# Kernel optimization log

Hardware: AMD Instinct MI355X
Metric: run time of the kernel (lower is better)

The kernel has to match this reference:

```python
import jax, jax.numpy as jnp
import numpy as np

N_SPACE = 197  # spatial tokens (ViT-B/16: 196 patches + CLS)
T = 8          # frames, fixed by space_time_pos shape (197*8, dim)
H = 12         # heads


def setup_inputs() -> dict:
    key = jax.random.key(0)
    ks = jax.random.split(key, 8)
    dim = 768
    B = 8
    Nq = 1576
    scale = dim ** -0.5
    return {
        "s_x": jax.random.normal(ks[0], (N_SPACE, B * T, dim), jnp.float32),
        "t_x": jax.random.normal(ks[1], (B, Nq, dim), jnp.float32),
        "space_time_pos": scale * jax.random.normal(ks[2], (N_SPACE * T, dim), jnp.float32),
        "q_w": jax.random.normal(ks[3], (dim, dim), jnp.float32) * 0.02,
        "q_b": jnp.zeros((dim,), jnp.float32),
        "kv_w": jax.random.normal(ks[4], (2 * dim, dim), jnp.float32) * 0.02,
        "kv_b": jnp.zeros((2 * dim,), jnp.float32),
        "proj_w": jax.random.normal(ks[5], (dim, dim), jnp.float32) * 0.02,
        "proj_b": jnp.zeros((dim,), jnp.float32),
    }


def reference(s_x, t_x, space_time_pos, q_w, q_b, kv_w, kv_b, proj_w, proj_b):
    n, BT, dim = s_x.shape
    B, Nq, _ = t_x.shape
    t = BT // B
    head_dim = dim // H
    scale = head_dim ** -0.5

    # rearrange 'n (b t) d -> b (t n) d'
    s = s_x.reshape(n, B, t, dim).transpose(1, 2, 0, 3).reshape(B, t * n, dim)
    s = s + space_time_pos  # (B, t*n, dim)

    # Q from t_x, K/V from s
    q = t_x @ q_w.T + q_b                      # (B, Nq, dim)
    kv = s @ kv_w.T + kv_b                     # (B, t*n, 2*dim)
    Nk = t * n
    # 'b n (e h d) -> e b h n d'
    kv = kv.reshape(B, Nk, 2, H, head_dim).transpose(2, 0, 3, 1, 4)
    k, v = kv[0], kv[1]                        # (B, H, Nk, hd)
    q = q.reshape(B, Nq, H, head_dim).transpose(0, 2, 1, 3) * scale  # (B, H, Nq, hd)

    attn = jnp.einsum('bhqd,bhkd->bhqk', q, k)
    attn = jax.nn.softmax(attn, axis=-1)
    out = jnp.einsum('bhqk,bhkd->bhqd', attn, v)   # (B, H, Nq, hd)
    out = out.transpose(0, 2, 1, 3).reshape(B, Nq, dim)
    return out @ proj_w.T + proj_b
```

## Files before the change

kernel.cpp:

```cpp
#include <hip/hip_runtime.h>
#include <stdint.h>

#define NSPACE 197
#define TFRAMES 8
#define NH 12
#define DIM 768
#define HD 64
#define BATCH 8
#define NQ 1576
#define NK 1576
#define M_REAL 12608
#define M_PAD 12672
#define VT_LD 1600

typedef __attribute__((ext_vector_type(8))) short s16x8;
typedef __attribute__((ext_vector_type(4))) short s16x4;
typedef __attribute__((ext_vector_type(4))) float f32x4;

__device__ inline uint16_t f2bf(float f) {
    union { float f; uint32_t i; } c; c.f = f;
    uint32_t r = c.i + 0x7FFF + ((c.i >> 16) & 1);
    return (uint16_t)(r >> 16);
}

__device__ inline uint32_t cvtpk_bf16(float lo, float hi) {
    uint32_t r;
    asm("v_cvt_pk_bf16_f32 %0, %1, %2" : "=v"(r) : "v"(lo), "v"(hi));
    return r;
}

__device__ inline float exp2_raw(float x) { return __builtin_amdgcn_exp2f(x); }

__device__ inline void gld_lds16(const uint16_t* g, uint16_t* l) {
    __builtin_amdgcn_global_load_lds(
        (const __attribute__((address_space(1))) void*)g,
        (__attribute__((address_space(3))) void*)l,
        16, 0, 0);
}

#define FILLB 4752
#define CONVQ_B 288
#define CONVKV_B 576
__global__ void prep(const float* __restrict__ t_x, const float* __restrict__ s_x,
                     const float* __restrict__ pos,
                     const float* __restrict__ q_w, const float* __restrict__ kv_w,
                     uint16_t* __restrict__ x_pad, uint16_t* __restrict__ s_pad,
                     uint16_t* __restrict__ wq, uint16_t* __restrict__ wkv) {
    int bx = blockIdx.x, tid = threadIdx.x;
    if (bx < FILLB) {
        int chunk = bx * 256 + tid;
        size_t off = (size_t)chunk * 8;
        s16x8 o;
        if (off < (size_t)M_REAL * DIM) {
            float4 a = *(const float4*)(t_x + off);
            float4 b = *(const float4*)(t_x + off + 4);
            union { s16x8 v; uint32_t u[4]; } p;
            p.u[0] = cvtpk_bf16(a.x, a.y);
            p.u[1] = cvtpk_bf16(a.z, a.w);
            p.u[2] = cvtpk_bf16(b.x, b.y);
            p.u[3] = cvtpk_bf16(b.z, b.w);
            o = p.v;
        } else {
            for (int j = 0; j < 8; j++) o[j] = 0;
        }
        *(s16x8*)(x_pad + off) = o;
    } else if (bx < 2 * FILLB) {
        int chunk = (bx - FILLB) * 256 + tid;
        int i = chunk / (DIM / 8);
        int cc = chunk - i * (DIM / 8);
        int d0 = cc * 8;
        uint16_t* dst = s_pad + (size_t)i * DIM + d0;
        if (i >= M_REAL) {
            s16x8 z; for (int j = 0; j < 8; j++) z[j] = 0;
            *(s16x8*)dst = z;
            return;
        }
        int b = i / NK, rr = i - b * NK;
        int t_i = rr / NSPACE, n_i = rr - t_i * NSPACE;
        const float* src = s_x + ((size_t)(n_i * (BATCH * TFRAMES) + b * TFRAMES + t_i)) * DIM + d0;
        const float* ps = pos + (size_t)rr * DIM + d0;
        float4 a0 = *(const float4*)src;
        float4 a1 = *(const float4*)(src + 4);
        float4 p0 = *(const float4*)ps;
        float4 p1 = *(const float4*)(ps + 4);
        union { s16x8 v; uint32_t u[4]; } o;
        o.u[0] = cvtpk_bf16(a0.x + p0.x, a0.y + p0.y);
        o.u[1] = cvtpk_bf16(a0.z + p0.z, a0.w + p0.w);
        o.u[2] = cvtpk_bf16(a1.x + p1.x, a1.y + p1.y);
        o.u[3] = cvtpk_bf16(a1.z + p1.z, a1.w + p1.w);
        *(s16x8*)dst = o.v;
    } else if (bx < 2 * FILLB + CONVQ_B) {
        int chunk = (bx - 2 * FILLB) * 256 + tid;
        size_t off = (size_t)chunk * 8;
        float4 a = *(const float4*)(q_w + off);
        float4 b = *(const float4*)(q_w + off + 4);
        union { s16x8 v; uint32_t u[4]; } o;
        o.u[0] = cvtpk_bf16(a.x, a.y);
        o.u[1] = cvtpk_bf16(a.z, a.w);
        o.u[2] = cvtpk_bf16(b.x, b.y);
        o.u[3] = cvtpk_bf16(b.z, b.w);
        *(s16x8*)(wq + off) = o.v;
    } else {
        int chunk = (bx - 2 * FILLB - CONVQ_B) * 256 + tid;
        size_t off = (size_t)chunk * 8;
        float4 a = *(const float4*)(kv_w + off);
        float4 b = *(const float4*)(kv_w + off + 4);
        union { s16x8 v; uint32_t u[4]; } o;
        o.u[0] = cvtpk_bf16(a.x, a.y);
        o.u[1] = cvtpk_bf16(a.z, a.w);
        o.u[2] = cvtpk_bf16(b.x, b.y);
        o.u[3] = cvtpk_bf16(b.z, b.w);
        *(s16x8*)(wkv + off) = o.v;
    }
}

__global__ void conv_f2b(const float* __restrict__ src, uint16_t* __restrict__ dst, int n8) {
    int chunk = blockIdx.x * 256 + threadIdx.x;
    if (chunk >= n8) return;
    size_t off = (size_t)chunk * 8;
    float4 a = *(const float4*)(src + off);
    float4 b = *(const float4*)(src + off + 4);
    union { s16x8 v; uint32_t u[4]; } o;
    o.u[0] = cvtpk_bf16(a.x, a.y);
    o.u[1] = cvtpk_bf16(a.z, a.w);
    o.u[2] = cvtpk_bf16(b.x, b.y);
    o.u[3] = cvtpk_bf16(b.z, b.w);
    *(s16x8*)(dst + off) = o.v;
}

template <int MODE>
__global__ __launch_bounds__(256)
void gemm_bt(const uint16_t* __restrict__ A, const uint16_t* __restrict__ W,
             const float* __restrict__ bias,
             uint16_t* __restrict__ out0, uint16_t* __restrict__ out1,
             float* __restrict__ outf) {
    __shared__ uint16_t As[128 * 32];
    __shared__ uint16_t Bs[128 * 32];
    const int t = threadIdx.x;
    const int lane = t & 63, w = t >> 6;
    const int r16 = lane & 15, quad = lane >> 4;
    const int wm = w >> 1, wn = w & 1;
    const int m0 = blockIdx.y * 128;
    const int n0 = blockIdx.x * 128;

    const int srow = w * 32 + (lane >> 2);
    const int scol = (lane & 3) * 8;
    const uint16_t* Ag = A + (size_t)(m0 + srow) * DIM + scol;
    const uint16_t* Wg = W + (size_t)(n0 + srow) * DIM + scol;
    uint16_t* Asw = &As[w * 32 * 32];
    uint16_t* Bsw = &Bs[w * 32 * 32];

    f32x4 acc[4][4];
    for (int a = 0; a < 4; a++)
        for (int bb = 0; bb < 4; bb++)
            for (int r = 0; r < 4; r++) acc[a][bb][r] = 0.f;

    for (int kk = 0; kk < DIM; kk += 32) {
        gld_lds16(Ag + kk, Asw);
        gld_lds16(Ag + kk + (size_t)16 * DIM, Asw + 16 * 32);
        gld_lds16(Wg + kk, Bsw);
        gld_lds16(Wg + kk + (size_t)16 * DIM, Bsw + 16 * 32);
        __syncthreads();
        s16x8 af[4], bfr[4];
        for (int mt = 0; mt < 4; mt++)
            af[mt] = *(const s16x8*)&As[(wm * 64 + mt * 16 + r16) * 32 + quad * 8];
        for (int nt = 0; nt < 4; nt++)
            bfr[nt] = *(const s16x8*)&Bs[(wn * 64 + nt * 16 + r16) * 32 + quad * 8];
        for (int mt = 0; mt < 4; mt++)
            for (int nt = 0; nt < 4; nt++)
                acc[mt][nt] = __builtin_amdgcn_mfma_f32_16x16x32_bf16(af[mt], bfr[nt], acc[mt][nt], 0, 0, 0);
        __syncthreads();
    }

    for (int mt = 0; mt < 4; mt++)
        for (int nt = 0; nt < 4; nt++) {
            int col = n0 + wn * 64 + nt * 16 + r16;
            float bz = bias[col];
            int rowb = m0 + wm * 64 + mt * 16 + quad * 4;
            for (int r = 0; r < 4; r++) {
                int i = rowb + r;
                if (i >= M_REAL) continue;
                float v = acc[mt][nt][r] + bz;
                if (MODE == 0) {
                    int b = i / NQ, nq = i - b * NQ;
                    int h = col >> 6, d = col & 63;
                    out0[(size_t)(((b * NH + h) * NQ) + nq) * HD + d] = f2bf(v * 0.18033688011112042f);
                } else if (MODE == 1) {
                    int b = i / NK, nk = i - b * NK;
                    if (col < DIM) {
                        int h = col >> 6, d = col & 63;
                        out0[(size_t)(((b * NH + h) * NK) + nk) * HD + d] = f2bf(v);
                    } else {
                        int c2 = col - DIM;
                        int h = c2 >> 6, d = c2 & 63;
                        out1[(size_t)(((b * NH + h) * NK) + nk) * HD + d] = f2bf(v);
                    }
                } else {
                    outf[(size_t)i * DIM + col] = v;
                }
            }
        }
}

__global__ __launch_bounds__(256)
void transpose_v(const uint16_t* __restrict__ v, uint16_t* __restrict__ vt) {
    __shared__ uint16_t T[64 * 72];
    int tile = blockIdx.x, bh = blockIdx.y;
    int nk0 = tile * 64;
    const uint16_t* V = v + (size_t)bh * NK * HD;
    uint16_t* VT = vt + (size_t)bh * HD * VT_LD;
    int tid = threadIdx.x;
    int rr = tid >> 3;
    int c8 = (tid & 7) * 8;
    for (int p = 0; p < 2; p++) {
        int lr = p * 32 + rr;
        int nk = nk0 + lr;
        s16x8 val;
        if (nk < NK) val = *(const s16x8*)(V + (size_t)nk * HD + c8);
        else for (int j = 0; j < 8; j++) val[j] = 0;
        for (int j = 0; j < 8; j++)
            T[(c8 + j) * 72 + lr] = (uint16_t)val[j];
    }
    __syncthreads();
    for (int p = 0; p < 2; p++) {
        int d = p * 32 + rr;
        s16x8 o = *(const s16x8*)&T[d * 72 + c8];
        *(s16x8*)(VT + (size_t)d * VT_LD + nk0 + c8) = o;
    }
}

#define NITER 50
__global__ __launch_bounds__(256)
void flash_attn(const uint16_t* __restrict__ q_buf, const uint16_t* __restrict__ k_buf,
                const uint16_t* __restrict__ vt_buf, uint16_t* __restrict__ ao) {
    __shared__ uint16_t Kb[2][32 * 72];
    __shared__ uint16_t Vb[2][64 * 40];
    int h = blockIdx.y, b = blockIdx.z;
    int tid = threadIdx.x;
    int lane = tid & 63, w = tid >> 6;
    int r16 = lane & 15, quad = lane >> 4;
    size_t bh = (size_t)(b * NH + h);
    const uint16_t* Q = q_buf + bh * NQ * HD;
    const uint16_t* K = k_buf + bh * NK * HD;
    const uint16_t* VT = vt_buf + bh * HD * VT_LD;
    int q0 = blockIdx.x * 128 + w * 32;

    const int kg = tid >> 3;
    const int kc = (tid & 7) * 8;
    const int kslot = ((kg >> 3) << 2) + (kg & 3) + ((kg & 4) ? 16 : 0);
    const int vd = tid >> 2;
    const int vc = (tid & 3) * 8;
    const uint16_t* Kg = K + (size_t)kg * HD + kc;
    const uint16_t* Vg = VT + (size_t)vd * VT_LD + vc;
    uint16_t* Kw = &Kb[0][kslot * 72 + kc];
    uint16_t* Vw = &Vb[0][vd * 40 + vc];
    const int KBSZ = 32 * 72, VBSZ = 64 * 40;

    s16x8 qf[2][2];
    for (int m = 0; m < 2; m++) {
        int qrow = q0 + m * 16 + r16;
        if (qrow < NQ) {
            qf[m][0] = *(const s16x8*)(Q + (size_t)qrow * HD + quad * 8);
            qf[m][1] = *(const s16x8*)(Q + (size_t)qrow * HD + 32 + quad * 8);
        } else {
            for (int j = 0; j < 8; j++) { qf[m][0][j] = 0; qf[m][1][j] = 0; }
        }
    }

    f32x4 z4;
    for (int r = 0; r < 4; r++) z4[r] = 0.f;
    s16x8 ones;
    for (int j = 0; j < 8; j++) ones[j] = (short)0x3F80;

    f32x4 oT[2][4];
    f32x4 oLs[2];
    for (int m = 0; m < 2; m++) {
        for (int dt = 0; dt < 4; dt++)
            for (int r = 0; r < 4; r++) oT[m][dt][r] = 0.f;
        for (int r = 0; r < 4; r++) oLs[m][r] = 0.f;
    }

    {
        s16x8 kv = *(const s16x8*)Kg;
        s16x8 vv = *(const s16x8*)Vg;
        *(s16x8*)Kw = kv;
        *(s16x8*)Vw = vv;
    }
    __syncthreads();

    for (int it = 0; it < NITER - 1; it++) {
        int kb = it * 32;
        int cur = it & 1, nxt = cur ^ 1;
        s16x8 knv = *(const s16x8*)(Kg + (size_t)(kb + 32) * HD);
        s16x8 vnv = *(const s16x8*)(Vg + kb + 32);

        const uint16_t* Kc = &Kb[cur][0];
        const uint16_t* Vc = &Vb[cur][0];
        s16x8 kfA0 = *(const s16x8*)(Kc + r16 * 72 + quad * 8);
        s16x8 kfA1 = *(const s16x8*)(Kc + r16 * 72 + 32 + quad * 8);
        s16x8 kfB0 = *(const s16x8*)(Kc + (16 + r16) * 72 + quad * 8);
        s16x8 kfB1 = *(const s16x8*)(Kc + (16 + r16) * 72 + 32 + quad * 8);

        s16x8 pf[2];
        #pragma unroll
        for (int m = 0; m < 2; m++) {
            f32x4 sA = __builtin_amdgcn_mfma_f32_16x16x32_bf16(kfA0, qf[m][0], z4, 0, 0, 0);
            sA = __builtin_amdgcn_mfma_f32_16x16x32_bf16(kfA1, qf[m][1], sA, 0, 0, 0);
            f32x4 sB = __builtin_amdgcn_mfma_f32_16x16x32_bf16(kfB0, qf[m][0], z4, 0, 0, 0);
            sB = __builtin_amdgcn_mfma_f32_16x16x32_bf16(kfB1, qf[m][1], sB, 0, 0, 0);
            f32x4 pA, pB;
            #pragma unroll
            for (int r = 0; r < 4; r++) { pA[r] = exp2_raw(sA[r]); pB[r] = exp2_raw(sB[r]); }
            union { s16x8 v; uint32_t u[4]; } pk;
            pk.u[0] = cvtpk_bf16(pA[0], pA[1]);
            pk.u[1] = cvtpk_bf16(pA[2], pA[3]);
            pk.u[2] = cvtpk_bf16(pB[0], pB[1]);
            pk.u[3] = cvtpk_bf16(pB[2], pB[3]);
            pf[m] = pk.v;
        }
        #pragma unroll
        for (int dt = 0; dt < 4; dt++) {
            s16x8 vf = *(const s16x8*)(Vc + (dt * 16 + r16) * 40 + quad * 8);
            oT[0][dt] = __builtin_amdgcn_mfma_f32_16x16x32_bf16(vf, pf[0], oT[0][dt], 0, 0, 0);
            oT[1][dt] = __builtin_amdgcn_mfma_f32_16x16x32_bf16(vf, pf[1], oT[1][dt], 0, 0, 0);
        }
        oLs[0] = __builtin_amdgcn_mfma_f32_16x16x32_bf16(ones, pf[0], oLs[0], 0, 0, 0);
        oLs[1] = __builtin_amdgcn_mfma_f32_16x16x32_bf16(ones, pf[1], oLs[1], 0, 0, 0);
        *(s16x8*)(Kw + nxt * KBSZ) = knv;
        *(s16x8*)(Vw + nxt * VBSZ) = vnv;
        __syncthreads();
    }

    {
        const int it = NITER - 1;
        const int kb = it * 32;
        const int cur = it & 1;
        const uint16_t* Kc = &Kb[cur][0];
        const uint16_t* Vc = &Vb[cur][0];
        s16x8 kfA0 = *(const s16x8*)(Kc + r16 * 72 + quad * 8);
        s16x8 kfA1 = *(const s16x8*)(Kc + r16 * 72 + 32 + quad * 8);
        s16x8 kfB0 = *(const s16x8*)(Kc + (16 + r16) * 72 + quad * 8);
        s16x8 kfB1 = *(const s16x8*)(Kc + (16 + r16) * 72 + 32 + quad * 8);

        s16x8 pf[2];
        #pragma unroll
        for (int m = 0; m < 2; m++) {
            f32x4 sA = __builtin_amdgcn_mfma_f32_16x16x32_bf16(kfA0, qf[m][0], z4, 0, 0, 0);
            sA = __builtin_amdgcn_mfma_f32_16x16x32_bf16(kfA1, qf[m][1], sA, 0, 0, 0);
            f32x4 sB = __builtin_amdgcn_mfma_f32_16x16x32_bf16(kfB0, qf[m][0], z4, 0, 0, 0);
            sB = __builtin_amdgcn_mfma_f32_16x16x32_bf16(kfB1, qf[m][1], sB, 0, 0, 0);
            f32x4 pA, pB;
            #pragma unroll
            for (int r = 0; r < 4; r++) {
                pA[r] = (kb + quad * 8 + r < NK)     ? exp2_raw(sA[r]) : 0.f;
                pB[r] = (kb + quad * 8 + 4 + r < NK) ? exp2_raw(sB[r]) : 0.f;
            }
            union { s16x8 v; uint32_t u[4]; } pk;
            pk.u[0] = cvtpk_bf16(pA[0], pA[1]);
            pk.u[1] = cvtpk_bf16(pA[2], pA[3]);
            pk.u[2] = cvtpk_bf16(pB[0], pB[1]);
            pk.u[3] = cvtpk_bf16(pB[2], pB[3]);
            pf[m] = pk.v;
        }
        #pragma unroll
        for (int dt = 0; dt < 4; dt++) {
            s16x8 vf = *(const s16x8*)(Vc + (dt * 16 + r16) * 40 + quad * 8);
            oT[0][dt] = __builtin_amdgcn_mfma_f32_16x16x32_bf16(vf, pf[0], oT[0][dt], 0, 0, 0);
            oT[1][dt] = __builtin_amdgcn_mfma_f32_16x16x32_bf16(vf, pf[1], oT[1][dt], 0, 0, 0);
        }
        oLs[0] = __builtin_amdgcn_mfma_f32_16x16x32_bf16(ones, pf[0], oLs[0], 0, 0, 0);
        oLs[1] = __builtin_amdgcn_mfma_f32_16x16x32_bf16(ones, pf[1], oLs[1], 0, 0, 0);
    }

    #pragma unroll
    for (int m = 0; m < 2; m++) {
        float rs = oLs[m][0];
        int q = q0 + m * 16 + r16;
        if (q >= NQ) continue;
        float inv = 1.0f / rs;
        size_t rowoff = (size_t)(b * NQ + q) * DIM + h * HD;
        #pragma unroll
        for (int dt = 0; dt < 4; dt++) {
            union { s16x4 v; uint32_t u[2]; } o;
            o.u[0] = cvtpk_bf16(oT[m][dt][0] * inv, oT[m][dt][1] * inv);
            o.u[1] = cvtpk_bf16(oT[m][dt][2] * inv, oT[m][dt][3] * inv);
            *(s16x4*)(ao + rowoff + dt * 16 + quad * 4) = o.v;
        }
    }
}

extern "C" void kernel_launch(void* const* d_in, const int* in_sizes, int n_in,
                              void* d_out, int out_size, void* d_ws, size_t ws_size,
                              hipStream_t stream) {
    const float* s_x    = (const float*)d_in[0];
    const float* t_x    = (const float*)d_in[1];
    const float* pos    = (const float*)d_in[2];
    const float* q_w    = (const float*)d_in[3];
    const float* q_b    = (const float*)d_in[4];
    const float* kv_w   = (const float*)d_in[5];
    const float* kv_b   = (const float*)d_in[6];
    const float* proj_w = (const float*)d_in[7];
    const float* proj_b = (const float*)d_in[8];
    float* out = (float*)d_out;

    char* ws = (char*)d_ws;
    size_t off = 0;
    auto carve = [&](size_t bytes) {
        void* p = ws + off;
        off += (bytes + 255) & ~(size_t)255;
        return p;
    };
    uint16_t* x_pad   = (uint16_t*)carve((size_t)M_PAD * DIM * 2);
    uint16_t* s_pad   = (uint16_t*)carve((size_t)M_PAD * DIM * 2);
    uint16_t* q_buf   = (uint16_t*)carve((size_t)BATCH * NH * NQ * HD * 2);
    uint16_t* k_buf   = (uint16_t*)carve((size_t)BATCH * NH * NK * HD * 2);
    uint16_t* vt_buf  = (uint16_t*)carve((size_t)BATCH * NH * HD * VT_LD * 2);
    uint16_t* wq_buf  = (uint16_t*)carve((size_t)DIM * DIM * 2);
    uint16_t* wkv_buf = (uint16_t*)carve((size_t)2 * DIM * DIM * 2);
    if (off > ws_size) return;
    uint16_t* v_buf = x_pad;
    uint16_t* ao    = x_pad;
    uint16_t* wproj = wq_buf;

    const int wq8 = DIM * DIM / 8;
    const int prep_blocks = 2 * FILLB + CONVQ_B + CONVKV_B;

    prep<<<prep_blocks, 256, 0, stream>>>(t_x, s_x, pos, q_w, kv_w,
                                          x_pad, s_pad, wq_buf, wkv_buf);

    gemm_bt<0><<<dim3(DIM / 128, M_PAD / 128), 256, 0, stream>>>(x_pad, wq_buf, q_b, q_buf, nullptr, nullptr);
    gemm_bt<1><<<dim3(2 * DIM / 128, M_PAD / 128), 256, 0, stream>>>(s_pad, wkv_buf, kv_b, k_buf, v_buf, nullptr);
    transpose_v<<<dim3(VT_LD / 64, BATCH * NH), 256, 0, stream>>>(v_buf, vt_buf);

    conv_f2b<<<(wq8 + 255) / 256, 256, 0, stream>>>(proj_w, wproj, wq8);

    flash_attn<<<dim3((NQ + 127) / 128, NH, BATCH), 256, 0, stream>>>(q_buf, k_buf, vt_buf, ao);

    gemm_bt<2><<<dim3(DIM / 128, M_PAD / 128), 256, 0, stream>>>(ao, wproj, proj_b, nullptr, nullptr, out);
}
```

Baseline: 360.9 us.

## Widen GEMM K-tile with XOR-swizzled LDS, remap attention blocks, drop ones-MFMA rowsum

The GEMM now stages a 64-wide K slice per iteration with an XOR-swizzled LDS layout. This halves the number of barriers and is meant to avoid LDS bank conflicts, at the cost of more shared memory per block. The attention kernel moves to a 1D grid that is remapped so neighbouring workgroups spread across XCDs in a chosen order. The row sum is now accumulated with vector adds plus cross-lane shuffles, replacing the extra MFMA against a ones vector. That trades some VALU work for fewer matrix instructions.

```diff
diff --git a/kernel.cpp b/kernel.cpp
--- a/kernel.cpp
+++ b/kernel.cpp
@@ -134,8 +134,8 @@
              const float* __restrict__ bias,
              uint16_t* __restrict__ out0, uint16_t* __restrict__ out1,
              float* __restrict__ outf) {
-    __shared__ uint16_t As[128 * 32];
-    __shared__ uint16_t Bs[128 * 32];
+    __shared__ uint16_t As[128 * 64];
+    __shared__ uint16_t Bs[128 * 64];
     const int t = threadIdx.x;
     const int lane = t & 63, w = t >> 6;
     const int r16 = lane & 15, quad = lane >> 4;
@@ -143,32 +143,40 @@
     const int m0 = blockIdx.y * 128;
     const int n0 = blockIdx.x * 128;
 
-    const int srow = w * 32 + (lane >> 2);
-    const int scol = (lane & 3) * 8;
-    const uint16_t* Ag = A + (size_t)(m0 + srow) * DIM + scol;
-    const uint16_t* Wg = W + (size_t)(n0 + srow) * DIM + scol;
-    uint16_t* Asw = &As[w * 32 * 32];
-    uint16_t* Bsw = &Bs[w * 32 * 32];
+    const int arow = lane >> 3;
+    const int achk = (lane & 7) ^ arow;
+    const uint16_t* Ag = A + (size_t)(m0 + w * 8 + arow) * DIM + achk * 8;
+    const uint16_t* Wg = W + (size_t)(n0 + w * 8 + arow) * DIM + achk * 8;
+    const int lb = (w * 8) * 64;
 
     f32x4 acc[4][4];
     for (int a = 0; a < 4; a++)
         for (int bb = 0; bb < 4; bb++)
             for (int r = 0; r < 4; r++) acc[a][bb][r] = 0.f;
 
-    for (int kk = 0; kk < DIM; kk += 32) {
-        gld_lds16(Ag + kk, Asw);
-        gld_lds16(Ag + kk + (size_t)16 * DIM, Asw + 16 * 32);
-        gld_lds16(Wg + kk, Bsw);
-        gld_lds16(Wg + kk + (size_t)16 * DIM, Bsw + 16 * 32);
+    for (int kk = 0; kk < DIM; kk += 64) {
+        #pragma unroll
+        for (int i = 0; i < 4; i++) {
+            gld_lds16(Ag + kk + (size_t)(i * 32) * DIM, &As[lb + i * 32 * 64]);
+            gld_lds16(Wg + kk + (size_t)(i * 32) * DIM, &Bs[lb + i * 32 * 64]);
+        }
         __syncthreads();
-        s16x8 af[4], bfr[4];
-        for (int mt = 0; mt < 4; mt++)
-            af[mt] = *(const s16x8*)&As[(wm * 64 + mt * 16 + r16) * 32 + quad * 8];
-        for (int nt = 0; nt < 4; nt++)
-            bfr[nt] = *(const s16x8*)&Bs[(wn * 64 + nt * 16 + r16) * 32 + quad * 8];
-        for (int mt = 0; mt < 4; mt++)
+        #pragma unroll
+        for (int hh = 0; hh < 2; hh++) {
+            const int pc = ((hh * 4 + quad) ^ (r16 & 7)) * 8;
+            s16x8 af[4], bfr[4];
+            #pragma unroll
+            for (int mt = 0; mt < 4; mt++)
+                af[mt] = *(const s16x8*)&As[(wm * 64 + mt * 16 + r16) * 64 + pc];
+            #pragma unroll
             for (int nt = 0; nt < 4; nt++)
-                acc[mt][nt] = __builtin_amdgcn_mfma_f32_16x16x32_bf16(af[mt], bfr[nt], acc[mt][nt], 0, 0, 0);
+                bfr[nt] = *(const s16x8*)&Bs[(wn * 64 + nt * 16 + r16) * 64 + pc];
+            #pragma unroll
+            for (int mt = 0; mt < 4; mt++)
+                #pragma unroll
+                for (int nt = 0; nt < 4; nt++)
+                    acc[mt][nt] = __builtin_amdgcn_mfma_f32_16x16x32_bf16(af[mt], bfr[nt], acc[mt][nt], 0, 0, 0);
+        }
         __syncthreads();
     }
 
@@ -230,12 +238,18 @@
 }
 
 #define NITER 50
+#define FLASH_WG 1248
 __global__ __launch_bounds__(256)
 void flash_attn(const uint16_t* __restrict__ q_buf, const uint16_t* __restrict__ k_buf,
                 const uint16_t* __restrict__ vt_buf, uint16_t* __restrict__ ao) {
     __shared__ uint16_t Kb[2][32 * 72];
     __shared__ uint16_t Vb[2][64 * 40];
-    int h = blockIdx.y, b = blockIdx.z;
+    int wgid = blockIdx.x;
+    int work = (wgid & 7) * (FLASH_WG / 8) + (wgid >> 3);
+    int qb = work % 13;
+    int hb = work / 13;
+    int h = hb % NH;
+    int b = hb / NH;
     int tid = threadIdx.x;
     int lane = tid & 63, w = tid >> 6;
     int r16 = lane & 15, quad = lane >> 4;
@@ -243,7 +257,7 @@
     const uint16_t* Q = q_buf + bh * NQ * HD;
     const uint16_t* K = k_buf + bh * NK * HD;
     const uint16_t* VT = vt_buf + bh * HD * VT_LD;
-    int q0 = blockIdx.x * 128 + w * 32;
+    int q0 = qb * 128 + w * 32;
 
     const int kg = tid >> 3;
     const int kc = (tid & 7) * 8;
@@ -269,15 +283,13 @@
 
     f32x4 z4;
     for (int r = 0; r < 4; r++) z4[r] = 0.f;
-    s16x8 ones;
-    for (int j = 0; j < 8; j++) ones[j] = (short)0x3F80;
 
     f32x4 oT[2][4];
-    f32x4 oLs[2];
+    f32x4 lsum4[2];
     for (int m = 0; m < 2; m++) {
         for (int dt = 0; dt < 4; dt++)
             for (int r = 0; r < 4; r++) oT[m][dt][r] = 0.f;
-        for (int r = 0; r < 4; r++) oLs[m][r] = 0.f;
+        for (int r = 0; r < 4; r++) lsum4[m][r] = 0.f;
     }
 
     {
@@ -311,6 +323,8 @@
             f32x4 pA, pB;
             #pragma unroll
             for (int r = 0; r < 4; r++) { pA[r] = exp2_raw(sA[r]); pB[r] = exp2_raw(sB[r]); }
+            lsum4[m] += pA;
+            lsum4[m] += pB;
             union { s16x8 v; uint32_t u[4]; } pk;
             pk.u[0] = cvtpk_bf16(pA[0], pA[1]);
             pk.u[1] = cvtpk_bf16(pA[2], pA[3]);
@@ -324,8 +338,6 @@
             oT[0][dt] = __builtin_amdgcn_mfma_f32_16x16x32_bf16(vf, pf[0], oT[0][dt], 0, 0, 0);
             oT[1][dt] = __builtin_amdgcn_mfma_f32_16x16x32_bf16(vf, pf[1], oT[1][dt], 0, 0, 0);
         }
-        oLs[0] = __builtin_amdgcn_mfma_f32_16x16x32_bf16(ones, pf[0], oLs[0], 0, 0, 0);
-        oLs[1] = __builtin_amdgcn_mfma_f32_16x16x32_bf16(ones, pf[1], oLs[1], 0, 0, 0);
         *(s16x8*)(Kw + nxt * KBSZ) = knv;
         *(s16x8*)(Vw + nxt * VBSZ) = vnv;
         __syncthreads();
@@ -355,6 +367,8 @@
                 pA[r] = (kb + quad * 8 + r < NK)     ? exp2_raw(sA[r]) : 0.f;
                 pB[r] = (kb + quad * 8 + 4 + r < NK) ? exp2_raw(sB[r]) : 0.f;
             }
+            lsum4[m] += pA;
+            lsum4[m] += pB;
             union { s16x8 v; uint32_t u[4]; } pk;
             pk.u[0] = cvtpk_bf16(pA[0], pA[1]);
             pk.u[1] = cvtpk_bf16(pA[2], pA[3]);
@@ -368,13 +382,13 @@
             oT[0][dt] = __builtin_amdgcn_mfma_f32_16x16x32_bf16(vf, pf[0], oT[0][dt], 0, 0, 0);
             oT[1][dt] = __builtin_amdgcn_mfma_f32_16x16x32_bf16(vf, pf[1], oT[1][dt], 0, 0, 0);
         }
-        oLs[0] = __builtin_amdgcn_mfma_f32_16x16x32_bf16(ones, pf[0], oLs[0], 0, 0, 0);
-        oLs[1] = __builtin_amdgcn_mfma_f32_16x16x32_bf16(ones, pf[1], oLs[1], 0, 0, 0);
     }
 
     #pragma unroll
     for (int m = 0; m < 2; m++) {
-        float rs = oLs[m][0];
+        float rs = lsum4[m][0] + lsum4[m][1] + lsum4[m][2] + lsum4[m][3];
+        rs += __shfl_xor(rs, 16);
+        rs += __shfl_xor(rs, 32);
         int q = q0 + m * 16 + r16;
         if (q >= NQ) continue;
         float inv = 1.0f / rs;
@@ -434,7 +448,7 @@
 
     conv_f2b<<<(wq8 + 255) / 256, 256, 0, stream>>>(proj_w, wproj, wq8);
 
-    flash_attn<<<dim3((NQ + 127) / 128, NH, BATCH), 256, 0, stream>>>(q_buf, k_buf, vt_buf, ao);
+    flash_attn<<<FLASH_WG, 256, 0, stream>>>(q_buf, k_buf, vt_buf, ao);
 
     gemm_bt<2><<<dim3(DIM / 128, M_PAD / 128), 256, 0, stream>>>(ao, wproj, proj_b, nullptr, nullptr, out);
 }
```

New measurement: 376.7 us. 1.04x slower.
